# Kernel tuning notes

Hardware: AMD Instinct MI355X
Metric: run time of the kernel (lower is better)

## Reference

```python
import jax, jax.numpy as jnp
import numpy as np

B, N, D = 2, 1024, 512
H, HD = 8, 64
RPE_IN, RPE_HID = 4, 64
FFN = 2048
EPS = 1e-5


def _layernorm(x, g, b):
    mu = jnp.mean(x, axis=-1, keepdims=True)
    var = jnp.var(x, axis=-1, keepdims=True)
    return (x - mu) * jax.lax.rsqrt(var + EPS) * g + b


def setup_inputs() -> dict:
    key = jax.random.key(0)
    ks = jax.random.split(key, 24)
    s = lambda fan_in: 1.0 / np.sqrt(fan_in)
    # weights stored [in, out] (torch Linear transposed)
    return {
        "x": jax.random.normal(ks[0], (B, N, D), jnp.float32),
        "rel_pos": jax.random.normal(ks[1], (B, N, N, RPE_IN), jnp.float32),
        "Wq": jax.random.uniform(ks[2], (D, D), jnp.float32, -s(D), s(D)),
        "bq": jnp.zeros((D,), jnp.float32),
        "Wk": jax.random.uniform(ks[3], (D, D), jnp.float32, -s(D), s(D)),
        "bk": jnp.zeros((D,), jnp.float32),
        "Wv": jax.random.uniform(ks[4], (D, D), jnp.float32, -s(D), s(D)),
        "bv": jnp.zeros((D,), jnp.float32),
        "Wo": jax.random.uniform(ks[5], (D, D), jnp.float32, -s(D), s(D)),
        "bo": jnp.zeros((D,), jnp.float32),
        "R1": jax.random.uniform(ks[6], (RPE_IN, RPE_HID), jnp.float32, -s(RPE_IN), s(RPE_IN)),
        "rb1": jnp.zeros((RPE_HID,), jnp.float32),
        "R2": jax.random.uniform(ks[7], (RPE_HID, H), jnp.float32, -s(RPE_HID), s(RPE_HID)),
        "rb2": jnp.zeros((H,), jnp.float32),
        "g1": jnp.ones((D,), jnp.float32),
        "b1": jnp.zeros((D,), jnp.float32),
        "g2": jnp.ones((D,), jnp.float32),
        "b2": jnp.zeros((D,), jnp.float32),
        "F1": jax.random.uniform(ks[8], (D, FFN), jnp.float32, -s(D), s(D)),
        "fb1": jnp.zeros((FFN,), jnp.float32),
        "F2": jax.random.uniform(ks[9], (FFN, D), jnp.float32, -s(FFN), s(FFN)),
        "fb2": jnp.zeros((D,), jnp.float32),
    }


def reference(x, rel_pos, Wq, bq, Wk, bk, Wv, bv, Wo, bo,
              R1, rb1, R2, rb2, g1, b1, g2, b2, F1, fb1, F2, fb2):
    scale = 1.0 / np.sqrt(HD)
    q = (x @ Wq + bq).reshape(B, N, H, HD).transpose(0, 2, 1, 3)  # [B,H,N,hd]
    k = (x @ Wk + bk).reshape(B, N, H, HD).transpose(0, 2, 1, 3)
    v = (x @ Wv + bv).reshape(B, N, H, HD).transpose(0, 2, 1, 3)
    attn = jnp.einsum('bhid,bhjd->bhij', q, k) * scale
    rpe = (jax.nn.relu(rel_pos @ R1 + rb1) @ R2 + rb2)  # [B,N,N,H]
    attn = attn + rpe.transpose(0, 3, 1, 2)
    attn = jax.nn.softmax(attn, axis=-1)
    out = jnp.einsum('bhij,bhjd->bhid', attn, v).transpose(0, 2, 1, 3).reshape(B, N, D)
    out = out @ Wo + bo
    x = _layernorm(x + out, g1, b1)
    ffn = jax.nn.gelu(x @ F1 + fb1, approximate=False) @ F2 + fb2
    return _layernorm(x + ffn, g2, b2)
```

## Files before the change

kernel.cpp:

```cpp
#include <hip/hip_runtime.h>
#include <math.h>

#define BATCH 2
#define SEQ   1024
#define DMODEL 512
#define NHEAD 8
#define HDIM  64
#define FFND  2048
#define BH    (BATCH*NHEAD)

typedef float  f32x4   __attribute__((ext_vector_type(4)));
typedef float  f32x16  __attribute__((ext_vector_type(16)));
typedef __bf16 bf16x8  __attribute__((ext_vector_type(8)));

#define WAITVM(n) asm volatile("s_waitcnt vmcnt(" #n ")" ::: "memory")

__device__ __forceinline__ unsigned short f2bf(float f) {
  union { __bf16 h; unsigned short u; } z; z.h = (__bf16)f; return z.u;
}
__device__ __forceinline__ float bf2f(unsigned short h) {
  union { unsigned u; float f; } x; x.u = ((unsigned)h) << 16;
  return x.f;
}
__device__ __forceinline__ unsigned pk2(float a, float b) {
  union { __bf16 h[2]; unsigned u; } z;
  z.h[0] = (__bf16)a; z.h[1] = (__bf16)b; return z.u;
}
__device__ __forceinline__ float gelu_f(float v) {
  float u = 0.7978845608f * (v + 0.044715f * v * v * v);
  float a = fabsf(u);
  float e = __expf(-2.f * a);
  float t = (1.f - e) / (1.f + e);
  t = copysignf(t, u);
  return 0.5f * v * (1.f + t);
}

__device__ __forceinline__ void load_lds16(const void* g, void* l) {
  __builtin_amdgcn_global_load_lds((const __attribute__((address_space(1))) void*)g,
                                   (__attribute__((address_space(3))) void*)l, 16, 0, 0);
}

__global__ __launch_bounds__(256) void prep_misc(
    const float* __restrict__ x, const float* __restrict__ bq,
    const float* __restrict__ bk, const float* __restrict__ bv,
    unsigned short* __restrict__ xb, float* __restrict__ bqkv) {
  int gid = blockIdx.x * 256 + threadIdx.x;
  float4 v = ((const float4*)x)[gid];
  ushort4 s;
  s.x = f2bf(v.x); s.y = f2bf(v.y); s.z = f2bf(v.z); s.w = f2bf(v.w);
  ((ushort4*)xb)[gid] = s;
  if (gid < 1536)
    bqkv[gid] = gid < 512 ? bq[gid] : (gid < 1024 ? bk[gid - 512] : bv[gid - 1024]);
}

__global__ __launch_bounds__(256) void prep_weights(
    const float* __restrict__ Wq, const float* __restrict__ Wk,
    const float* __restrict__ Wv, const float* __restrict__ Wo,
    const float* __restrict__ F1, const float* __restrict__ F2,
    unsigned short* __restrict__ qkvT, unsigned short* __restrict__ WoT,
    unsigned short* __restrict__ F1T, unsigned short* __restrict__ F2T) {
  __shared__ float t[32][33];
  int bid = blockIdx.x;
  const float* src; unsigned short* dst; int R, C, tx, ty;
  if (bid < 1024) {
    int m = bid >> 8;
    src = m == 0 ? Wq : m == 1 ? Wk : m == 2 ? Wv : Wo;
    dst = m < 3 ? qkvT + m * 512 * 512 : WoT;
    R = 512; C = 512; int u = bid & 255; tx = u & 15; ty = u >> 4;
  } else if (bid < 2048) {
    src = F1; dst = F1T; R = 512; C = 2048;
    int u = bid - 1024; tx = u & 63; ty = u >> 6;
  } else {
    src = F2; dst = F2T; R = 2048; C = 512;
    int u = bid - 2048; tx = u & 15; ty = u >> 4;
  }
  int c0 = tx * 32, r0 = ty * 32;
  int x_ = threadIdx.x, y_ = threadIdx.y;
#pragma unroll
  for (int i = 0; i < 4; i++)
    t[y_ + i * 8][x_] = src[(size_t)(r0 + y_ + i * 8) * C + c0 + x_];
  __syncthreads();
#pragma unroll
  for (int i = 0; i < 4; i++)
    dst[(size_t)(c0 + y_ + i * 8) * R + r0 + x_] = f2bf(t[x_][y_ + i * 8]);
}

__global__ __launch_bounds__(256) void rpe_mfma(
    const float* __restrict__ rel, const float* __restrict__ R1,
    const float* __restrict__ rb1, const float* __restrict__ R2,
    const float* __restrict__ rb2, unsigned short* __restrict__ rpe) {
  __shared__ unsigned short Hs[4][32 * 64];
  const int tid = threadIdx.x, lane = tid & 63, w = tid >> 6;
  const int l31 = lane & 31, hi = lane >> 5;
  const int l15 = lane & 15, l4g = lane >> 4;
  char* Hw = (char*)&Hs[w][0];

  bf16x8 a1[2];
#pragma unroll
  for (int mt = 0; mt < 2; mt++) {
    bf16x8 z = {};
    if (hi == 0) {
      int d = mt * 32 + l31;
      z[0] = (__bf16)R1[0 * 64 + d];
      z[1] = (__bf16)R1[1 * 64 + d];
      z[2] = (__bf16)R1[2 * 64 + d];
      z[3] = (__bf16)R1[3 * 64 + d];
      z[4] = (__bf16)rb1[d];
    }
    a1[mt] = z;
  }
  bf16x8 b2f[2];
#pragma unroll
  for (int ks = 0; ks < 2; ks++) {
    bf16x8 z = {};
    if (l15 < 8) {
#pragma unroll
      for (int j = 0; j < 8; j++)
        z[j] = (__bf16)R2[(ks * 32 + l4g * 8 + j) * 8 + l15];
    }
    b2f[ks] = z;
  }
  float rb2v = (l15 < 8) ? rb2[l15] : 0.f;

  const int wgid = blockIdx.x * 4 + w;
  float4 rv = {};
  if (hi == 0) rv = *(const float4*)&rel[(size_t)(wgid * 32 + l31) * 4];

  for (int c = 0; c < 8; c++) {
    int p0 = (wgid + c * 8192) * 32;
    float4 rc = rv;
    if (c < 7 && hi == 0)
      rv = *(const float4*)&rel[(size_t)((wgid + (c + 1) * 8192) * 32 + l31) * 4];

    bf16x8 b1 = {};
    if (hi == 0) {
      b1[0] = (__bf16)rc.x; b1[1] = (__bf16)rc.y;
      b1[2] = (__bf16)rc.z; b1[3] = (__bf16)rc.w;
      b1[4] = (__bf16)1.0f;
    }
    const int g1w = ((l31 & 7) ^ (l31 >> 3)) << 4;
#pragma unroll
    for (int mt = 0; mt < 2; mt++) {
      f32x16 hz = {};
      f32x16 h = __builtin_amdgcn_mfma_f32_32x32x16_bf16(a1[mt], b1, hz, 0, 0, 0);
#pragma unroll
      for (int q = 0; q < 4; q++) {
        float v0 = fmaxf(h[4 * q + 0], 0.f), v1 = fmaxf(h[4 * q + 1], 0.f);
        float v2 = fmaxf(h[4 * q + 2], 0.f), v3 = fmaxf(h[4 * q + 3], 0.f);
        uint2 pk; pk.x = pk2(v0, v1); pk.y = pk2(v2, v3);
        int byte = (l31 * 128 + mt * 64 + q * 16 + hi * 8) ^ g1w;
        *(uint2*)(Hw + byte) = pk;
      }
    }
    f32x4 acc2[2];
    acc2[0] = (f32x4){0.f, 0.f, 0.f, 0.f};
    acc2[1] = (f32x4){0.f, 0.f, 0.f, 0.f};
#pragma unroll
    for (int mt2 = 0; mt2 < 2; mt2++) {
      int row = mt2 * 16 + l15;
      int gr = ((row & 7) ^ (row >> 3)) << 4;
#pragma unroll
      for (int ks = 0; ks < 2; ks++) {
        int byte = row * 128 + (((ks * 4 + l4g) << 4) ^ gr);
        bf16x8 af = *(const bf16x8*)(Hw + byte);
        acc2[mt2] = __builtin_amdgcn_mfma_f32_16x16x32_bf16(af, b2f[ks], acc2[mt2], 0, 0, 0);
      }
    }
    if (l15 < 8) {
      int b = p0 >> 20, ij0 = (p0 & 1048575);
      size_t base = ((size_t)(b * 8 + l15) << 20) + ij0;
#pragma unroll
      for (int mt2 = 0; mt2 < 2; mt2++) {
        uint2 pk;
        pk.x = pk2(acc2[mt2][0] + rb2v, acc2[mt2][1] + rb2v);
        pk.y = pk2(acc2[mt2][2] + rb2v, acc2[mt2][3] + rb2v);
        *(uint2*)&rpe[base + mt2 * 16 + l4g * 4] = pk;
      }
    }
  }
}

enum { EPI_F32 = 0, EPI_GELU = 1, EPI_QKV = 2 };

template <int EPI, int BMt, int BNt, int WM, int WN>
__global__ __launch_bounds__(256) void gemm_bt(
    const unsigned short* __restrict__ A, const unsigned short* __restrict__ Bt,
    const float* __restrict__ bias, void* __restrict__ O0, void* __restrict__ O1,
    void* __restrict__ O2, int M, int N, int K) {
  __shared__ unsigned short As[2][BMt * 64];
  __shared__ unsigned short Bs[2][BNt * 64];
  const int tid = threadIdx.x, lane = tid & 63, w = tid >> 6;
  const int wr = w >> 1, wc = w & 1;
  const int m0 = blockIdx.y * BMt, n0 = blockIdx.x * BNt;
  const int l15 = lane & 15, l4g = lane >> 4;
  constexpr int NL = BMt / 32 + BNt / 32;

  f32x4 acc[WM][WN];
#pragma unroll
  for (int i = 0; i < WM; i++)
#pragma unroll
    for (int j = 0; j < WN; j++) acc[i][j] = (f32x4){0.f, 0.f, 0.f, 0.f};

  auto stage = [&](int buf, int kt) {
#pragma unroll
    for (int it = 0; it < BMt / 32; ++it) {
      int c = it * 256 + tid, row = c >> 3;
      int s16 = (c & 7) ^ (row & 7);
      load_lds16(A + (size_t)(m0 + row) * K + kt * 64 + s16 * 8,
                 (char*)&As[buf][0] + c * 16);
    }
#pragma unroll
    for (int it = 0; it < BNt / 32; ++it) {
      int c = it * 256 + tid, row = c >> 3;
      int s16 = (c & 7) ^ (row & 7);
      load_lds16(Bt + (size_t)(n0 + row) * K + kt * 64 + s16 * 8,
                 (char*)&Bs[buf][0] + c * 16);
    }
  };

  const int nkt = K / 64;
  stage(0, 0);
  for (int kt = 0; kt < nkt; ++kt) {
    const int cur = kt & 1;
    if (kt + 1 < nkt) {
      stage(cur ^ 1, kt + 1);
      if constexpr (NL == 6) WAITVM(6); else WAITVM(4);
    } else {
      WAITVM(0);
    }
    __builtin_amdgcn_s_barrier();
#pragma unroll
    for (int kk = 0; kk < 2; ++kk) {
      bf16x8 af[WM], bfv[WN];
#pragma unroll
      for (int i = 0; i < WM; i++) {
        int row = wr * (WM * 16) + i * 16 + l15;
        af[i] = *(const bf16x8*)((char*)&As[cur][0] + row * 128 +
                                 (((kk * 4 + l4g) ^ (row & 7)) << 4));
      }
#pragma unroll
      for (int j = 0; j < WN; j++) {
        int row = wc * (WN * 16) + j * 16 + l15;
        bfv[j] = *(const bf16x8*)((char*)&Bs[cur][0] + row * 128 +
                                  (((kk * 4 + l4g) ^ (row & 7)) << 4));
      }
#pragma unroll
      for (int i = 0; i < WM; i++)
#pragma unroll
        for (int j = 0; j < WN; j++)
          acc[i][j] = __builtin_amdgcn_mfma_f32_16x16x32_bf16(af[i], bfv[j], acc[i][j], 0, 0, 0);
    }
    if (kt + 1 < nkt) {
      asm volatile("" ::: "memory");
      __builtin_amdgcn_s_barrier();
    }
  }

#pragma unroll
  for (int i = 0; i < WM; i++) {
    int row = m0 + wr * (WM * 16) + i * 16 + l4g * 4;
#pragma unroll
    for (int j = 0; j < WN; j++) {
      int col = n0 + wc * (WN * 16) + j * 16 + l15;
      float bv = bias ? bias[col] : 0.f;
#pragma unroll
      for (int r = 0; r < 4; r++) {
        float v = acc[i][j][r] + bv;
        int rr = row + r;
        if (EPI == EPI_F32) {
          ((float*)O0)[(size_t)rr * N + col] = v;
        } else if (EPI == EPI_GELU) {
          ((unsigned short*)O0)[(size_t)rr * N + col] = f2bf(gelu_f(v));
        } else {
          int b = rr >> 10, n = rr & 1023;
          int d = col & 511, h = d >> 6, hd = d & 63;
          int bh = b * 8 + h;
          unsigned short bv16 = f2bf(v);
          if (col < 512)
            ((unsigned short*)O0)[((size_t)bh * 1024 + n) * 64 + hd] = bv16;
          else if (col < 1024)
            ((unsigned short*)O1)[((size_t)bh * 1024 + n) * 64 + hd] = bv16;
          else
            ((unsigned short*)O2)[((size_t)bh * 64 + hd) * 1024 + n] = bv16;
        }
      }
    }
  }
}

__global__ __launch_bounds__(128) void attn_kernel(
    const unsigned short* __restrict__ Qh, const unsigned short* __restrict__ Kh,
    const unsigned short* __restrict__ VT, const unsigned short* __restrict__ rpe,
    unsigned short* __restrict__ AO) {
  __shared__ unsigned short Ks[2][64 * 64], Vs[2][64 * 64];
  __shared__ unsigned short Rs[2][32 * 64];
  __shared__ unsigned short Ps[2][16 * 64];
  const int tid = threadIdx.x, lane = tid & 63, w = tid >> 6;
  const int l15 = lane & 15, l4g = lane >> 4;
  const int bid = blockIdx.x;
  const int it = (bid >> 3) & 31;
  const int bh = (bid & 7) | (((bid >> 8) & 1) << 3);
  const int i0 = it * 32;
  const unsigned short* Qb = Qh + (size_t)bh * SEQ * HDIM;
  const unsigned short* Kb = Kh + (size_t)bh * SEQ * HDIM;
  const unsigned short* Vb = VT + (size_t)bh * HDIM * SEQ;
  const unsigned short* Rb = rpe + ((size_t)bh << 20);

  bf16x8 qf[2];
#pragma unroll
  for (int kk = 0; kk < 2; kk++)
    qf[kk] = *(const bf16x8*)&Qb[(size_t)(i0 + w * 16 + l15) * 64 + kk * 32 + l4g * 8];

  f32x4 o[4];
#pragma unroll
  for (int i = 0; i < 4; i++) o[i] = (f32x4){0.f, 0.f, 0.f, 0.f};
  float m4[4], l4s[4];
#pragma unroll
  for (int r = 0; r < 4; r++) { m4[r] = -1e30f; l4s[r] = 0.f; }

  auto stage = [&](int buf, int jt) {
    int j0 = jt * 64;
#pragma unroll
    for (int itn = 0; itn < 4; ++itn) {
      int c = itn * 128 + tid, row = c >> 3;
      int s8 = ((c & 7) ^ (row & 7)) * 8;
      load_lds16(Kb + (size_t)(j0 + row) * 64 + s8, (char*)&Ks[buf][0] + c * 16);
    }
#pragma unroll
    for (int itn = 0; itn < 4; ++itn) {
      int c = itn * 128 + tid, row = c >> 3;
      int s8 = ((c & 7) ^ (row & 7)) * 8;
      load_lds16(Vb + (size_t)row * SEQ + j0 + s8, (char*)&Vs[buf][0] + c * 16);
    }
#pragma unroll
    for (int itn = 0; itn < 2; ++itn) {
      int c = itn * 128 + tid, row = c >> 3;
      int s8 = ((c & 7) ^ (row & 7)) * 8;
      load_lds16(Rb + (size_t)(i0 + row) * SEQ + j0 + s8, (char*)&Rs[buf][0] + c * 16);
    }
  };

  stage(0, 0);
  for (int jt = 0; jt < 16; ++jt) {
    const int cur = jt & 1;
    if (jt < 15) {
      stage(cur ^ 1, jt + 1);
      WAITVM(10);
    } else {
      WAITVM(0);
    }
    __builtin_amdgcn_s_barrier();

    f32x4 sa[4];
#pragma unroll
    for (int js = 0; js < 4; js++) sa[js] = (f32x4){0.f, 0.f, 0.f, 0.f};
    __builtin_amdgcn_s_setprio(1);
#pragma unroll
    for (int kk = 0; kk < 2; kk++) {
#pragma unroll
      for (int js = 0; js < 4; js++) {
        int row = js * 16 + l15;
        bf16x8 kb = *(const bf16x8*)((char*)&Ks[cur][0] + row * 128 +
                                     (((kk * 4 + l4g) ^ (row & 7)) << 4));
        sa[js] = __builtin_amdgcn_mfma_f32_16x16x32_bf16(qf[kk], kb, sa[js], 0, 0, 0);
      }
    }
    __builtin_amdgcn_s_setprio(0);
    float p[4][4], mx[4];
#pragma unroll
    for (int r = 0; r < 4; r++) mx[r] = -1e30f;
#pragma unroll
    for (int js = 0; js < 4; js++)
#pragma unroll
      for (int r = 0; r < 4; r++) {
        int row = w * 16 + l4g * 4 + r;
        int byte = row * 128 + ((((js * 2) + (l15 >> 3)) ^ (row & 7)) << 4) + ((l15 & 7) << 1);
        float rv = bf2f(*(const unsigned short*)((const char*)&Rs[cur][0] + byte));
        float s = sa[js][r] * 0.125f + rv;
        p[js][r] = s;
        mx[r] = fmaxf(mx[r], s);
      }
#pragma unroll
    for (int off = 1; off < 16; off <<= 1)
#pragma unroll
      for (int r = 0; r < 4; r++) mx[r] = fmaxf(mx[r], __shfl_xor(mx[r], off));
    float al[4], sm[4];
#pragma unroll
    for (int r = 0; r < 4; r++) {
      float nm = fmaxf(m4[r], mx[r]);
      al[r] = __expf(m4[r] - nm);
      m4[r] = nm;
      sm[r] = 0.f;
    }
#pragma unroll
    for (int js = 0; js < 4; js++)
#pragma unroll
      for (int r = 0; r < 4; r++) {
        float e = __expf(p[js][r] - m4[r]);
        p[js][r] = e;
        sm[r] += e;
      }
#pragma unroll
    for (int off = 1; off < 16; off <<= 1)
#pragma unroll
      for (int r = 0; r < 4; r++) sm[r] += __shfl_xor(sm[r], off);
#pragma unroll
    for (int r = 0; r < 4; r++) l4s[r] = l4s[r] * al[r] + sm[r];
#pragma unroll
    for (int hdf = 0; hdf < 4; hdf++)
#pragma unroll
      for (int r = 0; r < 4; r++) o[hdf][r] *= al[r];
#pragma unroll
    for (int js = 0; js < 4; js++)
#pragma unroll
      for (int r = 0; r < 4; r++) {
        int row = l4g * 4 + r;
        int byte = row * 128 + ((((js * 2) + (l15 >> 3)) ^ (row & 7)) << 4) + ((l15 & 7) << 1);
        *(unsigned short*)((char*)&Ps[w][0] + byte) = f2bf(p[js][r]);
      }
    __builtin_amdgcn_s_setprio(1);
#pragma unroll
    for (int kk = 0; kk < 2; kk++) {
      bf16x8 pf = *(const bf16x8*)((char*)&Ps[w][0] + l15 * 128 +
                                   (((kk * 4 + l4g) ^ (l15 & 7)) << 4));
#pragma unroll
      for (int hdf = 0; hdf < 4; hdf++) {
        int row = hdf * 16 + l15;
        bf16x8 vb = *(const bf16x8*)((char*)&Vs[cur][0] + row * 128 +
                                     (((kk * 4 + l4g) ^ (row & 7)) << 4));
        o[hdf] = __builtin_amdgcn_mfma_f32_16x16x32_bf16(pf, vb, o[hdf], 0, 0, 0);
      }
    }
    __builtin_amdgcn_s_setprio(0);
    if (jt < 15) {
      asm volatile("" ::: "memory");
      __builtin_amdgcn_s_barrier();
    }
  }
  const int b = bh >> 3, h = bh & 7;
#pragma unroll
  for (int hdf = 0; hdf < 4; hdf++)
#pragma unroll
    for (int r = 0; r < 4; r++) {
      float v = o[hdf][r] / l4s[r];
      int n = i0 + w * 16 + l4g * 4 + r;
      AO[((size_t)b * SEQ + n) * DMODEL + h * 64 + hdf * 16 + l15] = f2bf(v);
    }
}

__global__ __launch_bounds__(256) void ln_kernel(
    const float* __restrict__ a, const float* __restrict__ res,
    const float* __restrict__ g, const float* __restrict__ be,
    float* __restrict__ outf, unsigned short* __restrict__ outb) {
  const int row = blockIdx.x, t = threadIdx.x;
  const float* pa = a + (size_t)row * DMODEL;
  const float* pb = res + (size_t)row * DMODEL;
  float v0 = pa[t] + pb[t];
  float v1 = pa[t + 256] + pb[t + 256];
  float s = v0 + v1, sq = v0 * v0 + v1 * v1;
#pragma unroll
  for (int off = 1; off < 64; off <<= 1) {
    s += __shfl_xor(s, off);
    sq += __shfl_xor(sq, off);
  }
  __shared__ float ls[4], lq[4];
  int w = t >> 6, lane = t & 63;
  if (lane == 0) { ls[w] = s; lq[w] = sq; }
  __syncthreads();
  s = ls[0] + ls[1] + ls[2] + ls[3];
  sq = lq[0] + lq[1] + lq[2] + lq[3];
  float mu = s * (1.f / DMODEL);
  float var = sq * (1.f / DMODEL) - mu * mu;
  float rs = rsqrtf(var + 1e-5f);
  float y0 = (v0 - mu) * rs * g[t] + be[t];
  float y1v = (v1 - mu) * rs * g[t + 256] + be[t + 256];
  outf[(size_t)row * DMODEL + t] = y0;
  outf[(size_t)row * DMODEL + t + 256] = y1v;
  if (outb) {
    outb[(size_t)row * DMODEL + t] = f2bf(y0);
    outb[(size_t)row * DMODEL + t + 256] = f2bf(y1v);
  }
}

extern "C" void kernel_launch(void* const* d_in, const int* in_sizes, int n_in,
                              void* d_out, int out_size, void* d_ws, size_t ws_size,
                              hipStream_t stream) {
  const float* x   = (const float*)d_in[0];
  const float* rel = (const float*)d_in[1];
  const float* Wq  = (const float*)d_in[2];
  const float* bq  = (const float*)d_in[3];
  const float* Wk  = (const float*)d_in[4];
  const float* bk  = (const float*)d_in[5];
  const float* Wv  = (const float*)d_in[6];
  const float* bv  = (const float*)d_in[7];
  const float* Wo  = (const float*)d_in[8];
  const float* bo  = (const float*)d_in[9];
  const float* R1  = (const float*)d_in[10];
  const float* rb1 = (const float*)d_in[11];
  const float* R2  = (const float*)d_in[12];
  const float* rb2 = (const float*)d_in[13];
  const float* g1  = (const float*)d_in[14];
  const float* b1  = (const float*)d_in[15];
  const float* g2  = (const float*)d_in[16];
  const float* b2  = (const float*)d_in[17];
  const float* F1  = (const float*)d_in[18];
  const float* fb1 = (const float*)d_in[19];
  const float* F2  = (const float*)d_in[20];
  const float* fb2 = (const float*)d_in[21];

  char* p = (char*)d_ws;
  auto alloc = [&](size_t bytes) {
    char* r = p;
    p += (bytes + 255) & ~(size_t)255;
    return r;
  };
  unsigned short* xb   = (unsigned short*)alloc((size_t)2048 * 512 * 2);
  unsigned short* qkvT = (unsigned short*)alloc((size_t)1536 * 512 * 2);
  float*          bqkv = (float*)alloc(1536 * 4);
  unsigned short* WoT  = (unsigned short*)alloc((size_t)512 * 512 * 2);
  unsigned short* F1T  = (unsigned short*)alloc((size_t)2048 * 512 * 2);
  unsigned short* F2T  = (unsigned short*)alloc((size_t)512 * 2048 * 2);
  unsigned short* Qhp  = (unsigned short*)alloc((size_t)BH * SEQ * HDIM * 2);
  unsigned short* Khp  = (unsigned short*)alloc((size_t)BH * SEQ * HDIM * 2);
  unsigned short* VTp  = (unsigned short*)alloc((size_t)BH * HDIM * SEQ * 2);
  unsigned short* rpep = (unsigned short*)alloc((size_t)BH * SEQ * SEQ * 2);
  unsigned short* attO = (unsigned short*)alloc((size_t)2048 * 512 * 2);
  float*          t1   = (float*)alloc((size_t)2048 * 512 * 4);
  float*          y1   = (float*)alloc((size_t)2048 * 512 * 4);
  unsigned short* y1b  = (unsigned short*)alloc((size_t)2048 * 512 * 2);
  float*          t2   = t1;
  unsigned short* hbuf = rpep;

  prep_misc<<<1024, 256, 0, stream>>>(x, bq, bk, bv, xb, bqkv);
  prep_weights<<<3072, dim3(32, 8), 0, stream>>>(Wq, Wk, Wv, Wo, F1, F2,
                                                 qkvT, WoT, F1T, F2T);
  rpe_mfma<<<2048, 256, 0, stream>>>(rel, R1, rb1, R2, rb2, rpep);

  gemm_bt<EPI_QKV, 128, 64, 4, 2><<<dim3(24, 16), 256, 0, stream>>>(
      xb, qkvT, bqkv, Qhp, Khp, VTp, 2048, 1536, 512);
  attn_kernel<<<512, 128, 0, stream>>>(Qhp, Khp, VTp, rpep, attO);

  gemm_bt<EPI_F32, 64, 64, 2, 2><<<dim3(8, 32), 256, 0, stream>>>(
      attO, WoT, bo, t1, nullptr, nullptr, 2048, 512, 512);
  ln_kernel<<<2048, 256, 0, stream>>>(x, t1, g1, b1, y1, y1b);

  gemm_bt<EPI_GELU, 128, 64, 4, 2><<<dim3(32, 16), 256, 0, stream>>>(
      y1b, F1T, fb1, hbuf, nullptr, nullptr, 2048, 2048, 512);
  gemm_bt<EPI_F32, 64, 64, 2, 2><<<dim3(8, 32), 256, 0, stream>>>(
      hbuf, F2T, fb2, t2, nullptr, nullptr, 2048, 512, 2048);
  ln_kernel<<<2048, 256, 0, stream>>>(y1, t2, g2, b2, (float*)d_out, nullptr);
}
```

Baseline: 248.4 us.

## Split attention over KV halves, drop online max, fold log2e into RPE

The attention kernel now handles 64 query rows per 256-thread block. Each block covers only half of the key/value sequence (split-KV). It writes unnormalized fp32 partial outputs and row sums, and a new combine kernel adds the two halves and normalizes to bf16. The online-softmax running max and rescaling are removed and exp2f is used directly. The log2e factor is prefolded into the RPE MLP weights and the score scale. This cuts per-tile reduction work and doubles the parallelism per head, but adds an extra kernel and an fp32 round trip. Without max subtraction the exponentials can overflow for large logits, and the partial-output buffer aliases past t1 into the adjacent allocation.

```diff
diff --git a/kernel.cpp b/kernel.cpp
--- a/kernel.cpp
+++ b/kernel.cpp
@@ -93,6 +93,7 @@
   const int tid = threadIdx.x, lane = tid & 63, w = tid >> 6;
   const int l31 = lane & 31, hi = lane >> 5;
   const int l15 = lane & 15, l4g = lane >> 4;
+  const float LOG2E = 1.4426950408889634f;
   char* Hw = (char*)&Hs[w][0];
 
   bf16x8 a1[2];
@@ -116,11 +117,11 @@
     if (l15 < 8) {
 #pragma unroll
       for (int j = 0; j < 8; j++)
-        z[j] = (__bf16)R2[(ks * 32 + l4g * 8 + j) * 8 + l15];
+        z[j] = (__bf16)(R2[(ks * 32 + l4g * 8 + j) * 8 + l15] * LOG2E);
     }
     b2f[ks] = z;
   }
-  float rb2v = (l15 < 8) ? rb2[l15] : 0.f;
+  float rb2v = (l15 < 8) ? rb2[l15] * LOG2E : 0.f;
 
   const int wgid = blockIdx.x * 4 + w;
   float4 rv = {};
@@ -288,23 +289,25 @@
   }
 }
 
-__global__ __launch_bounds__(128) void attn_kernel(
+__global__ __launch_bounds__(256, 2) void attn_kernel(
     const unsigned short* __restrict__ Qh, const unsigned short* __restrict__ Kh,
     const unsigned short* __restrict__ VT, const unsigned short* __restrict__ rpe,
-    unsigned short* __restrict__ AO) {
-  __shared__ unsigned short Ks[2][64 * 64], Vs[2][64 * 64];
-  __shared__ unsigned short Rs[2][32 * 64];
-  __shared__ unsigned short Ps[2][16 * 64];
+    float* __restrict__ oP, float* __restrict__ lP) {
+  __shared__ unsigned short Ks[2][64 * 64], Vs[2][64 * 64], Rs[2][64 * 64];
+  __shared__ unsigned short Ps[4][16 * 64];
   const int tid = threadIdx.x, lane = tid & 63, w = tid >> 6;
   const int l15 = lane & 15, l4g = lane >> 4;
   const int bid = blockIdx.x;
-  const int it = (bid >> 3) & 31;
-  const int bh = (bid & 7) | (((bid >> 8) & 1) << 3);
-  const int i0 = it * 32;
+  const int it = (bid >> 3) & 15;
+  const int bh = (bid & 7) | (((bid >> 7) & 1) << 3);
+  const int kv = (bid >> 8) & 1;
+  const int i0 = it * 64;
+  const float C = 0.18033688011112042f;
   const unsigned short* Qb = Qh + (size_t)bh * SEQ * HDIM;
   const unsigned short* Kb = Kh + (size_t)bh * SEQ * HDIM;
   const unsigned short* Vb = VT + (size_t)bh * HDIM * SEQ;
   const unsigned short* Rb = rpe + ((size_t)bh << 20);
+  char* Pw = (char*)&Ps[w][0];
 
   bf16x8 qf[2];
 #pragma unroll
@@ -314,38 +317,26 @@
   f32x4 o[4];
 #pragma unroll
   for (int i = 0; i < 4; i++) o[i] = (f32x4){0.f, 0.f, 0.f, 0.f};
-  float m4[4], l4s[4];
-#pragma unroll
-  for (int r = 0; r < 4; r++) { m4[r] = -1e30f; l4s[r] = 0.f; }
+  float lsum = 0.f;
 
   auto stage = [&](int buf, int jt) {
     int j0 = jt * 64;
 #pragma unroll
-    for (int itn = 0; itn < 4; ++itn) {
-      int c = itn * 128 + tid, row = c >> 3;
+    for (int itn = 0; itn < 2; ++itn) {
+      int c = itn * 256 + tid, row = c >> 3;
       int s8 = ((c & 7) ^ (row & 7)) * 8;
       load_lds16(Kb + (size_t)(j0 + row) * 64 + s8, (char*)&Ks[buf][0] + c * 16);
-    }
-#pragma unroll
-    for (int itn = 0; itn < 4; ++itn) {
-      int c = itn * 128 + tid, row = c >> 3;
-      int s8 = ((c & 7) ^ (row & 7)) * 8;
       load_lds16(Vb + (size_t)row * SEQ + j0 + s8, (char*)&Vs[buf][0] + c * 16);
-    }
-#pragma unroll
-    for (int itn = 0; itn < 2; ++itn) {
-      int c = itn * 128 + tid, row = c >> 3;
-      int s8 = ((c & 7) ^ (row & 7)) * 8;
       load_lds16(Rb + (size_t)(i0 + row) * SEQ + j0 + s8, (char*)&Rs[buf][0] + c * 16);
     }
   };
 
-  stage(0, 0);
-  for (int jt = 0; jt < 16; ++jt) {
-    const int cur = jt & 1;
-    if (jt < 15) {
-      stage(cur ^ 1, jt + 1);
-      WAITVM(10);
+  stage(0, kv * 8);
+  for (int jtl = 0; jtl < 8; ++jtl) {
+    const int cur = jtl & 1;
+    if (jtl < 7) {
+      stage(cur ^ 1, kv * 8 + jtl + 1);
+      WAITVM(6);
     } else {
       WAITVM(0);
     }
@@ -362,90 +353,69 @@
         int row = js * 16 + l15;
         bf16x8 kb = *(const bf16x8*)((char*)&Ks[cur][0] + row * 128 +
                                      (((kk * 4 + l4g) ^ (row & 7)) << 4));
-        sa[js] = __builtin_amdgcn_mfma_f32_16x16x32_bf16(qf[kk], kb, sa[js], 0, 0, 0);
+        sa[js] = __builtin_amdgcn_mfma_f32_16x16x32_bf16(kb, qf[kk], sa[js], 0, 0, 0);
       }
     }
     __builtin_amdgcn_s_setprio(0);
-    float p[4][4], mx[4];
-#pragma unroll
-    for (int r = 0; r < 4; r++) mx[r] = -1e30f;
-#pragma unroll
-    for (int js = 0; js < 4; js++)
-#pragma unroll
-      for (int r = 0; r < 4; r++) {
-        int row = w * 16 + l4g * 4 + r;
-        int byte = row * 128 + ((((js * 2) + (l15 >> 3)) ^ (row & 7)) << 4) + ((l15 & 7) << 1);
-        float rv = bf2f(*(const unsigned short*)((const char*)&Rs[cur][0] + byte));
-        float s = sa[js][r] * 0.125f + rv;
-        p[js][r] = s;
-        mx[r] = fmaxf(mx[r], s);
-      }
-#pragma unroll
-    for (int off = 1; off < 16; off <<= 1)
-#pragma unroll
-      for (int r = 0; r < 4; r++) mx[r] = fmaxf(mx[r], __shfl_xor(mx[r], off));
-    float al[4], sm[4];
-#pragma unroll
-    for (int r = 0; r < 4; r++) {
-      float nm = fmaxf(m4[r], mx[r]);
-      al[r] = __expf(m4[r] - nm);
-      m4[r] = nm;
-      sm[r] = 0.f;
-    }
-#pragma unroll
-    for (int js = 0; js < 4; js++)
-#pragma unroll
-      for (int r = 0; r < 4; r++) {
-        float e = __expf(p[js][r] - m4[r]);
-        p[js][r] = e;
-        sm[r] += e;
-      }
-#pragma unroll
-    for (int off = 1; off < 16; off <<= 1)
-#pragma unroll
-      for (int r = 0; r < 4; r++) sm[r] += __shfl_xor(sm[r], off);
-#pragma unroll
-    for (int r = 0; r < 4; r++) l4s[r] = l4s[r] * al[r] + sm[r];
-#pragma unroll
-    for (int hdf = 0; hdf < 4; hdf++)
-#pragma unroll
-      for (int r = 0; r < 4; r++) o[hdf][r] *= al[r];
-#pragma unroll
-    for (int js = 0; js < 4; js++)
-#pragma unroll
-      for (int r = 0; r < 4; r++) {
-        int row = l4g * 4 + r;
-        int byte = row * 128 + ((((js * 2) + (l15 >> 3)) ^ (row & 7)) << 4) + ((l15 & 7) << 1);
-        *(unsigned short*)((char*)&Ps[w][0] + byte) = f2bf(p[js][r]);
-      }
+
+    const int rrow = w * 16 + l15;
+    const int rswz = (rrow & 7) << 4;
+    const int pswz = (l15 & 7) << 4;
+#pragma unroll
+    for (int js = 0; js < 4; js++) {
+      int rbyte = rrow * 128 + ((((js * 2) + (l4g >> 1)) << 4) ^ rswz) + ((l4g & 1) << 3);
+      uint2 rv2 = *(const uint2*)((const char*)&Rs[cur][0] + rbyte);
+      float p0 = exp2f(sa[js][0] * C + bf2f((unsigned short)(rv2.x & 0xffff)));
+      float p1 = exp2f(sa[js][1] * C + bf2f((unsigned short)(rv2.x >> 16)));
+      float p2 = exp2f(sa[js][2] * C + bf2f((unsigned short)(rv2.y & 0xffff)));
+      float p3 = exp2f(sa[js][3] * C + bf2f((unsigned short)(rv2.y >> 16)));
+      lsum += (p0 + p1) + (p2 + p3);
+      uint2 pk; pk.x = pk2(p0, p1); pk.y = pk2(p2, p3);
+      *(uint2*)(Pw + l15 * 128 + (((js * 32 + l4g * 8)) ^ pswz)) = pk;
+    }
+
     __builtin_amdgcn_s_setprio(1);
 #pragma unroll
     for (int kk = 0; kk < 2; kk++) {
-      bf16x8 pf = *(const bf16x8*)((char*)&Ps[w][0] + l15 * 128 +
-                                   (((kk * 4 + l4g) ^ (l15 & 7)) << 4));
+      bf16x8 pf = *(const bf16x8*)(Pw + l15 * 128 + ((kk * 64 + l4g * 16) ^ pswz));
 #pragma unroll
       for (int hdf = 0; hdf < 4; hdf++) {
         int row = hdf * 16 + l15;
         bf16x8 vb = *(const bf16x8*)((char*)&Vs[cur][0] + row * 128 +
                                      (((kk * 4 + l4g) ^ (row & 7)) << 4));
-        o[hdf] = __builtin_amdgcn_mfma_f32_16x16x32_bf16(pf, vb, o[hdf], 0, 0, 0);
+        o[hdf] = __builtin_amdgcn_mfma_f32_16x16x32_bf16(vb, pf, o[hdf], 0, 0, 0);
       }
     }
     __builtin_amdgcn_s_setprio(0);
-    if (jt < 15) {
+    if (jtl < 7) {
       asm volatile("" ::: "memory");
       __builtin_amdgcn_s_barrier();
     }
   }
+
+  lsum += __shfl_xor(lsum, 16);
+  lsum += __shfl_xor(lsum, 32);
+
   const int b = bh >> 3, h = bh & 7;
+  const int nrow = b * SEQ + i0 + w * 16 + l15;
 #pragma unroll
   for (int hdf = 0; hdf < 4; hdf++)
-#pragma unroll
-    for (int r = 0; r < 4; r++) {
-      float v = o[hdf][r] / l4s[r];
-      int n = i0 + w * 16 + l4g * 4 + r;
-      AO[((size_t)b * SEQ + n) * DMODEL + h * 64 + hdf * 16 + l15] = f2bf(v);
-    }
+    *(f32x4*)&oP[(size_t)kv * 2048 * 512 + (size_t)nrow * 512 +
+                 h * 64 + hdf * 16 + l4g * 4] = o[hdf];
+  if (l4g == 0)
+    lP[kv * 16384 + bh * 1024 + i0 + w * 16 + l15] = lsum;
+}
+
+__global__ __launch_bounds__(256) void attn_combine(
+    const float* __restrict__ oP, const float* __restrict__ lP,
+    unsigned short* __restrict__ AO) {
+  const int n = blockIdx.x, t = threadIdx.x;
+  float2 a = *(const float2*)&oP[(size_t)n * 512 + t * 2];
+  float2 c = *(const float2*)&oP[(size_t)(2048 + n) * 512 + t * 2];
+  int bh = (n >> 10) * 8 + (t >> 5), nq = n & 1023;
+  float l = lP[bh * 1024 + nq] + lP[16384 + bh * 1024 + nq];
+  float inv = 1.f / l;
+  ((unsigned*)AO)[(size_t)n * 256 + t] = pk2((a.x + c.x) * inv, (a.y + c.y) * inv);
 }
 
 __global__ __launch_bounds__(256) void ln_kernel(
@@ -530,6 +500,8 @@
   unsigned short* y1b  = (unsigned short*)alloc((size_t)2048 * 512 * 2);
   float*          t2   = t1;
   unsigned short* hbuf = rpep;
+  float*          oP   = t1;
+  float*          lP   = (float*)y1b;
 
   prep_misc<<<1024, 256, 0, stream>>>(x, bq, bk, bv, xb, bqkv);
   prep_weights<<<3072, dim3(32, 8), 0, stream>>>(Wq, Wk, Wv, Wo, F1, F2,
@@ -538,7 +510,8 @@
 
   gemm_bt<EPI_QKV, 128, 64, 4, 2><<<dim3(24, 16), 256, 0, stream>>>(
       xb, qkvT, bqkv, Qhp, Khp, VTp, 2048, 1536, 512);
-  attn_kernel<<<512, 128, 0, stream>>>(Qhp, Khp, VTp, rpep, attO);
+  attn_kernel<<<512, 256, 0, stream>>>(Qhp, Khp, VTp, rpep, oP, lP);
+  attn_combine<<<2048, 256, 0, stream>>>(oP, lP, attO);
 
   gemm_bt<EPI_F32, 64, 64, 2, 2><<<dim3(8, 32), 256, 0, stream>>>(
       attO, WoT, bo, t1, nullptr, nullptr, 2048, 512, 512);
```

Result: faster. 234.5 us (-5.6%).
